# Performance work log

Measured on AMD Instinct MI355X. Metric: run time of the kernel, lower is better.

## Reference

```python
import jax, jax.numpy as jnp
import numpy as np

B, NQ, NK, D, DV = 16, 2048, 2048, 128, 128


def setup_inputs() -> dict:
    key = jax.random.key(0)
    kq, kk, kv, kl = jax.random.split(key, 4)
    return {
        "queries": jax.random.normal(kq, (B, NQ, D), dtype=jnp.float32),
        "keys": jax.random.normal(kk, (B, NK, D), dtype=jnp.float32),
        "values": jax.random.normal(kv, (B, NK, DV), dtype=jnp.float32),
        "valid_lens": jax.random.randint(kl, (B,), 1, NK + 1, dtype=jnp.int32),
    }


def reference(queries, keys, values, valid_lens):
    d = queries.shape[-1]
    # scores: [B, NQ, NK]
    scores = jnp.einsum("bqd,bkd->bqk", queries, keys) / jnp.sqrt(jnp.float32(d))
    # mask positions >= valid_len with -1e6 (matches sequence_mask semantics)
    key_pos = jnp.arange(scores.shape[-1], dtype=jnp.int32)  # [NK]
    mask = key_pos[None, None, :] < valid_lens[:, None, None]  # [B,1,NK] -> broadcast over queries
    scores = jnp.where(mask, scores, jnp.float32(-1000000.0))
    attn = jax.nn.softmax(scores, axis=-1)
    # dropout p=0.0 -> identity
    return jnp.einsum("bqk,bkv->bqv", attn, values)
```

## Files before the change

### kernel.cpp

```cpp
#include <hip/hip_runtime.h>


#define B_   16
#define NQ_  2048
#define NK_  2048
#define D_   128
#define DV_  128

typedef __attribute__((ext_vector_type(4))) float          f32x4;
typedef __attribute__((ext_vector_type(8))) __bf16         bf16x8;
typedef __attribute__((ext_vector_type(8))) unsigned short ushort8v;
typedef __attribute__((ext_vector_type(4))) unsigned short ushort4v;

__device__ __forceinline__ unsigned short f2bf(float f) {
    unsigned u = __builtin_bit_cast(unsigned, f);
    return (unsigned short)((u + 0x8000u) >> 16);
}
__device__ __forceinline__ float bf2f(unsigned short h) {
    unsigned u = ((unsigned)h) << 16;
    return __builtin_bit_cast(float, u);
}

__global__ __launch_bounds__(256, 2) void attn_fwd(
    const float* __restrict__ Q, const float* __restrict__ K,
    const float* __restrict__ V, const int* __restrict__ vlen,
    float* __restrict__ Out)
{
    __shared__ unsigned short Kt[64][136];
    __shared__ unsigned short Vt[128 * 64];
    __shared__ unsigned short Pb[4][16][72];

    const int tid  = threadIdx.x;
    const int w    = tid >> 6;
    const int L    = tid & 63;
    const int col  = L & 15;
    const int quad = L >> 4;
    const int b     = blockIdx.y;
    const int qbase = blockIdx.x * 64;
    const int vl    = vlen[b];
    const int ntiles = (vl + 63) >> 6;

    const float qscale = 0.12751743f;
    bf16x8 qf[4];
    {
        const int qrow = qbase + w * 16 + col;
        const float* gQ = Q + ((size_t)b * NQ_ + qrow) * D_;
        #pragma unroll
        for (int c = 0; c < 4; ++c) {
            const float* p = gQ + c * 32 + quad * 8;
            f32x4 a0 = *(const f32x4*)(p);
            f32x4 a1 = *(const f32x4*)(p + 4);
            ushort8v us;
            us[0] = f2bf(a0[0] * qscale); us[1] = f2bf(a0[1] * qscale);
            us[2] = f2bf(a0[2] * qscale); us[3] = f2bf(a0[3] * qscale);
            us[4] = f2bf(a1[0] * qscale); us[5] = f2bf(a1[1] * qscale);
            us[6] = f2bf(a1[2] * qscale); us[7] = f2bf(a1[3] * qscale);
            qf[c] = __builtin_bit_cast(bf16x8, us);
        }
    }

    f32x4 o[8];
    #pragma unroll
    for (int c = 0; c < 8; ++c) o[c] = (f32x4){0.f, 0.f, 0.f, 0.f};
    float m_run[4] = {-1e30f, -1e30f, -1e30f, -1e30f};
    float l_run[4] = {0.f, 0.f, 0.f, 0.f};

    const float* gKb = K + (size_t)b * NK_ * D_;
    const float* gVb = V + (size_t)b * NK_ * DV_;

    f32x4 kreg[8];
    float vreg[4][8];

    #define ISSUE_LOADS(K0)                                                  \
        do {                                                                 \
            _Pragma("unroll")                                                \
            for (int i = 0; i < 8; ++i) {                                    \
                int f = i * 256 + tid;                                       \
                int row = f >> 5, c4 = (f & 31) * 4;                         \
                kreg[i] = *(const f32x4*)(gKb + (size_t)((K0) + row) * D_ + c4); \
            }                                                                \
            _Pragma("unroll")                                                \
            for (int i = 0; i < 4; ++i) {                                    \
                int item = i * 256 + tid;                                    \
                int dv = item & 127, kg = item >> 7;                         \
                const float* vp = gVb + (size_t)((K0) + kg * 8) * DV_ + dv;  \
                _Pragma("unroll")                                            \
                for (int j = 0; j < 8; ++j) vreg[i][j] = vp[(size_t)j * DV_];\
            }                                                                \
        } while (0)

    ISSUE_LOADS(0);

    for (int kt = 0; kt < ntiles; ++kt) {
        __syncthreads();

        #pragma unroll
        for (int i = 0; i < 8; ++i) {
            int f = i * 256 + tid;
            int row = f >> 5, c4 = (f & 31) * 4;
            ushort4v ks;
            ks[0] = f2bf(kreg[i][0]); ks[1] = f2bf(kreg[i][1]);
            ks[2] = f2bf(kreg[i][2]); ks[3] = f2bf(kreg[i][3]);
            *(ushort4v*)&Kt[row][c4] = ks;
        }
        #pragma unroll
        for (int i = 0; i < 4; ++i) {
            int item = i * 256 + tid;
            int dv = item & 127, kg = item >> 7;
            ushort8v us;
            #pragma unroll
            for (int j = 0; j < 8; ++j) us[j] = f2bf(vreg[i][j]);
            *(ushort8v*)&Vt[dv * 64 + (((kg ^ (dv & 7))) << 3)] = us;
        }

        if (kt + 1 < ntiles) ISSUE_LOADS((kt + 1) * 64);

        __syncthreads();

        const int k0 = kt * 64;

        f32x4 s[4];
        #pragma unroll
        for (int kc = 0; kc < 4; ++kc) {
            f32x4 acc = (f32x4){0.f, 0.f, 0.f, 0.f};
            const unsigned short* krow = &Kt[kc * 16 + col][quad * 8];
            #pragma unroll
            for (int c = 0; c < 4; ++c) {
                bf16x8 kb = __builtin_bit_cast(bf16x8, *(const ushort8v*)(krow + c * 32));
                acc = __builtin_amdgcn_mfma_f32_16x16x32_bf16(qf[c], kb, acc, 0, 0, 0);
            }
            s[kc] = acc;
        }

        if (k0 + 64 > vl) {
            #pragma unroll
            for (int kc = 0; kc < 4; ++kc)
                if (k0 + kc * 16 + col >= vl)
                    s[kc] = (f32x4){-1e30f, -1e30f, -1e30f, -1e30f};
        }

        float mx[4];
        #pragma unroll
        for (int r = 0; r < 4; ++r)
            mx[r] = fmaxf(fmaxf(s[0][r], s[1][r]), fmaxf(s[2][r], s[3][r]));
        #pragma unroll
        for (int off = 1; off < 16; off <<= 1) {
            #pragma unroll
            for (int r = 0; r < 4; ++r)
                mx[r] = fmaxf(mx[r], __shfl_xor(mx[r], off, 64));
        }

        f32x4 al;
        #pragma unroll
        for (int r = 0; r < 4; ++r) {
            float mn = fmaxf(m_run[r], mx[r]);
            al[r] = exp2f(m_run[r] - mn);
            m_run[r] = mn;
        }

        float rs[4] = {0.f, 0.f, 0.f, 0.f};
        #pragma unroll
        for (int kc = 0; kc < 4; ++kc) {
            #pragma unroll
            for (int r = 0; r < 4; ++r) {
                unsigned short pb = f2bf(exp2f(s[kc][r] - m_run[r]));
                Pb[w][quad * 4 + r][kc * 16 + col] = pb;
                rs[r] += bf2f(pb);
            }
        }
        #pragma unroll
        for (int off = 1; off < 16; off <<= 1) {
            #pragma unroll
            for (int r = 0; r < 4; ++r)
                rs[r] += __shfl_xor(rs[r], off, 64);
        }
        #pragma unroll
        for (int r = 0; r < 4; ++r)
            l_run[r] = l_run[r] * al[r] + rs[r];
        #pragma unroll
        for (int c = 0; c < 8; ++c) o[c] *= al;


        #pragma unroll
        for (int kc2 = 0; kc2 < 2; ++kc2) {
            bf16x8 pa = __builtin_bit_cast(bf16x8,
                *(const ushort8v*)&Pb[w][col][kc2 * 32 + quad * 8]);
            #pragma unroll
            for (int c = 0; c < 8; ++c) {
                int dv = c * 16 + col;
                int sw = ((kc2 * 4 + quad) ^ (col & 7)) << 3;
                bf16x8 vb = __builtin_bit_cast(bf16x8,
                    *(const ushort8v*)&Vt[dv * 64 + sw]);
                o[c] = __builtin_amdgcn_mfma_f32_16x16x32_bf16(pa, vb, o[c], 0, 0, 0);
            }
        }
    }

    f32x4 linv;
    #pragma unroll
    for (int r = 0; r < 4; ++r) linv[r] = 1.0f / l_run[r];
    float* gO = Out + ((size_t)b * NQ_ + qbase + w * 16) * DV_;
    #pragma unroll
    for (int c = 0; c < 8; ++c) {
        #pragma unroll
        for (int r = 0; r < 4; ++r)
            gO[(size_t)(quad * 4 + r) * DV_ + c * 16 + col] = o[c][r] * linv[r];
    }
    #undef ISSUE_LOADS
}

extern "C" void kernel_launch(void* const* d_in, const int* in_sizes, int n_in,
                              void* d_out, int out_size, void* d_ws, size_t ws_size,
                              hipStream_t stream) {
    const float* Q  = (const float*)d_in[0];
    const float* K  = (const float*)d_in[1];
    const float* V  = (const float*)d_in[2];
    const int*   vl = (const int*)d_in[3];
    float* out = (float*)d_out;
    dim3 grid(NQ_ / 64, B_, 1);
    attn_fwd<<<grid, dim3(256, 1, 1), 0, stream>>>(Q, K, V, vl, out);
}
```

Baseline: 154.7 us.

## Split KV range across two blocks per query tile with flag-based merge

```diff
diff --git a/kernel.cpp b/kernel.cpp
--- a/kernel.cpp
+++ b/kernel.cpp
@@ -6,11 +6,21 @@
 #define NK_  2048
 #define D_   128
 #define DV_  128
+#define NQT_ 32
+#define NPAIR_ (B_ * NQT_)
+#define KHALF_TILES 16
 
 typedef __attribute__((ext_vector_type(4))) float          f32x4;
 typedef __attribute__((ext_vector_type(8))) __bf16         bf16x8;
 typedef __attribute__((ext_vector_type(8))) unsigned short ushort8v;
-typedef __attribute__((ext_vector_type(4))) unsigned short ushort4v;
+typedef __attribute__((ext_vector_type(2))) unsigned int   uint2v;
+typedef __attribute__((ext_vector_type(4))) unsigned int   uint4v;
+
+#ifdef __has_builtin
+#if __has_builtin(__builtin_amdgcn_cvt_pk_bf16_f32)
+#define HAVE_CVT_PK_BF16 1
+#endif
+#endif
 
 __device__ __forceinline__ unsigned short f2bf(float f) {
     unsigned u = __builtin_bit_cast(unsigned, f);
@@ -20,44 +30,44 @@
     unsigned u = ((unsigned)h) << 16;
     return __builtin_bit_cast(float, u);
 }
-
-__global__ __launch_bounds__(256, 2) void attn_fwd(
+__device__ __forceinline__ unsigned f2bf2(float a, float b) {
+#ifdef HAVE_CVT_PK_BF16
+    auto t = __builtin_amdgcn_cvt_pk_bf16_f32(a, b);
+    return __builtin_bit_cast(unsigned, t);
+#else
+    return (unsigned)f2bf(a) | ((unsigned)f2bf(b) << 16);
+#endif
+}
+
+__global__ void init_flags(int* __restrict__ f) { f[threadIdx.x] = 0; }
+
+__global__ __launch_bounds__(256, 3) void attn_fwd(
     const float* __restrict__ Q, const float* __restrict__ K,
     const float* __restrict__ V, const int* __restrict__ vlen,
-    float* __restrict__ Out)
+    float* __restrict__ Out, int* __restrict__ flags,
+    float* __restrict__ mlbuf, unsigned short* __restrict__ obuf)
 {
     __shared__ unsigned short Kt[64][136];
     __shared__ unsigned short Vt[128 * 64];
     __shared__ unsigned short Pb[4][16][72];
+    __shared__ int s_old;
 
     const int tid  = threadIdx.x;
     const int w    = tid >> 6;
     const int L    = tid & 63;
     const int col  = L & 15;
     const int quad = L >> 4;
-    const int b     = blockIdx.y;
-    const int qbase = blockIdx.x * 64;
+
+    const int id   = blockIdx.x;
+    const int h    = id >> 9;
+    const int pid  = id & 511;
+    const int b    = pid & 15;
+    const int qt   = pid >> 4;
+    const int qbase = qt * 64;
     const int vl    = vlen[b];
     const int ntiles = (vl + 63) >> 6;
-
-    const float qscale = 0.12751743f;
-    bf16x8 qf[4];
-    {
-        const int qrow = qbase + w * 16 + col;
-        const float* gQ = Q + ((size_t)b * NQ_ + qrow) * D_;
-        #pragma unroll
-        for (int c = 0; c < 4; ++c) {
-            const float* p = gQ + c * 32 + quad * 8;
-            f32x4 a0 = *(const f32x4*)(p);
-            f32x4 a1 = *(const f32x4*)(p + 4);
-            ushort8v us;
-            us[0] = f2bf(a0[0] * qscale); us[1] = f2bf(a0[1] * qscale);
-            us[2] = f2bf(a0[2] * qscale); us[3] = f2bf(a0[3] * qscale);
-            us[4] = f2bf(a1[0] * qscale); us[5] = f2bf(a1[1] * qscale);
-            us[6] = f2bf(a1[2] * qscale); us[7] = f2bf(a1[3] * qscale);
-            qf[c] = __builtin_bit_cast(bf16x8, us);
-        }
-    }
+    const int t0 = h * KHALF_TILES;
+    const int t1 = ntiles < (h + 1) * KHALF_TILES ? ntiles : (h + 1) * KHALF_TILES;
 
     f32x4 o[8];
     #pragma unroll
@@ -65,148 +75,210 @@
     float m_run[4] = {-1e30f, -1e30f, -1e30f, -1e30f};
     float l_run[4] = {0.f, 0.f, 0.f, 0.f};
 
-    const float* gKb = K + (size_t)b * NK_ * D_;
-    const float* gVb = V + (size_t)b * NK_ * DV_;
-
-    f32x4 kreg[8];
-    float vreg[4][8];
-
-    #define ISSUE_LOADS(K0)                                                  \
-        do {                                                                 \
-            _Pragma("unroll")                                                \
-            for (int i = 0; i < 8; ++i) {                                    \
-                int f = i * 256 + tid;                                       \
-                int row = f >> 5, c4 = (f & 31) * 4;                         \
-                kreg[i] = *(const f32x4*)(gKb + (size_t)((K0) + row) * D_ + c4); \
-            }                                                                \
-            _Pragma("unroll")                                                \
-            for (int i = 0; i < 4; ++i) {                                    \
-                int item = i * 256 + tid;                                    \
-                int dv = item & 127, kg = item >> 7;                         \
-                const float* vp = gVb + (size_t)((K0) + kg * 8) * DV_ + dv;  \
-                _Pragma("unroll")                                            \
-                for (int j = 0; j < 8; ++j) vreg[i][j] = vp[(size_t)j * DV_];\
-            }                                                                \
-        } while (0)
-
-    ISSUE_LOADS(0);
-
-    for (int kt = 0; kt < ntiles; ++kt) {
-        __syncthreads();
-
-        #pragma unroll
-        for (int i = 0; i < 8; ++i) {
-            int f = i * 256 + tid;
-            int row = f >> 5, c4 = (f & 31) * 4;
-            ushort4v ks;
-            ks[0] = f2bf(kreg[i][0]); ks[1] = f2bf(kreg[i][1]);
-            ks[2] = f2bf(kreg[i][2]); ks[3] = f2bf(kreg[i][3]);
-            *(ushort4v*)&Kt[row][c4] = ks;
-        }
-        #pragma unroll
-        for (int i = 0; i < 4; ++i) {
-            int item = i * 256 + tid;
-            int dv = item & 127, kg = item >> 7;
-            ushort8v us;
-            #pragma unroll
-            for (int j = 0; j < 8; ++j) us[j] = f2bf(vreg[i][j]);
-            *(ushort8v*)&Vt[dv * 64 + (((kg ^ (dv & 7))) << 3)] = us;
-        }
-
-        if (kt + 1 < ntiles) ISSUE_LOADS((kt + 1) * 64);
-
-        __syncthreads();
-
-        const int k0 = kt * 64;
-
-        f32x4 s[4];
-        #pragma unroll
-        for (int kc = 0; kc < 4; ++kc) {
-            f32x4 acc = (f32x4){0.f, 0.f, 0.f, 0.f};
-            const unsigned short* krow = &Kt[kc * 16 + col][quad * 8];
+    if (t0 < t1) {
+        const float qscale = 0.12751743f;
+        bf16x8 qf[4];
+        {
+            const int qrow = qbase + w * 16 + col;
+            const float* gQ = Q + ((size_t)b * NQ_ + qrow) * D_;
             #pragma unroll
             for (int c = 0; c < 4; ++c) {
-                bf16x8 kb = __builtin_bit_cast(bf16x8, *(const ushort8v*)(krow + c * 32));
-                acc = __builtin_amdgcn_mfma_f32_16x16x32_bf16(qf[c], kb, acc, 0, 0, 0);
-            }
-            s[kc] = acc;
-        }
-
-        if (k0 + 64 > vl) {
-            #pragma unroll
-            for (int kc = 0; kc < 4; ++kc)
-                if (k0 + kc * 16 + col >= vl)
-                    s[kc] = (f32x4){-1e30f, -1e30f, -1e30f, -1e30f};
-        }
-
-        float mx[4];
-        #pragma unroll
-        for (int r = 0; r < 4; ++r)
-            mx[r] = fmaxf(fmaxf(s[0][r], s[1][r]), fmaxf(s[2][r], s[3][r]));
-        #pragma unroll
-        for (int off = 1; off < 16; off <<= 1) {
+                const float* p = gQ + c * 32 + quad * 8;
+                f32x4 a0 = *(const f32x4*)(p);
+                f32x4 a1 = *(const f32x4*)(p + 4);
+                uint4v us;
+                us[0] = f2bf2(a0[0] * qscale, a0[1] * qscale);
+                us[1] = f2bf2(a0[2] * qscale, a0[3] * qscale);
+                us[2] = f2bf2(a1[0] * qscale, a1[1] * qscale);
+                us[3] = f2bf2(a1[2] * qscale, a1[3] * qscale);
+                qf[c] = __builtin_bit_cast(bf16x8, us);
+            }
+        }
+
+        const float* gKb = K + (size_t)b * NK_ * D_;
+        const float* gVb = V + (size_t)b * NK_ * DV_;
+
+        f32x4 kreg[8];
+        float vreg[4][8];
+
+        #define ISSUE_LOADS(K0)                                                  \
+            do {                                                                 \
+                _Pragma("unroll")                                                \
+                for (int i = 0; i < 8; ++i) {                                    \
+                    int f = i * 256 + tid;                                       \
+                    int row = f >> 5, c4 = (f & 31) * 4;                         \
+                    kreg[i] = *(const f32x4*)(gKb + (size_t)((K0) + row) * D_ + c4); \
+                }                                                                \
+                _Pragma("unroll")                                                \
+                for (int i = 0; i < 4; ++i) {                                    \
+                    int item = i * 256 + tid;                                    \
+                    int dv = item & 127, kg = item >> 7;                         \
+                    const float* vp = gVb + (size_t)((K0) + kg * 8) * DV_ + dv;  \
+                    _Pragma("unroll")                                            \
+                    for (int j = 0; j < 8; ++j) vreg[i][j] = vp[(size_t)j * DV_];\
+                }                                                                \
+            } while (0)
+
+        ISSUE_LOADS(t0 * 64);
+
+        for (int kt = t0; kt < t1; ++kt) {
+            __syncthreads();
+
+            #pragma unroll
+            for (int i = 0; i < 8; ++i) {
+                int f = i * 256 + tid;
+                int row = f >> 5, c4 = (f & 31) * 4;
+                uint2v ks;
+                ks[0] = f2bf2(kreg[i][0], kreg[i][1]);
+                ks[1] = f2bf2(kreg[i][2], kreg[i][3]);
+                *(uint2v*)&Kt[row][c4] = ks;
+            }
+            #pragma unroll
+            for (int i = 0; i < 4; ++i) {
+                int item = i * 256 + tid;
+                int dv = item & 127, kg = item >> 7;
+                uint4v us;
+                us[0] = f2bf2(vreg[i][0], vreg[i][1]);
+                us[1] = f2bf2(vreg[i][2], vreg[i][3]);
+                us[2] = f2bf2(vreg[i][4], vreg[i][5]);
+                us[3] = f2bf2(vreg[i][6], vreg[i][7]);
+                *(uint4v*)&Vt[dv * 64 + ((kg ^ (dv & 7)) << 3)] = us;
+            }
+
+            if (kt + 1 < t1) ISSUE_LOADS((kt + 1) * 64);
+
+            __syncthreads();
+
+            const int k0 = kt * 64;
+
+            f32x4 s[4];
+            #pragma unroll
+            for (int kc = 0; kc < 4; ++kc) {
+                f32x4 acc = (f32x4){0.f, 0.f, 0.f, 0.f};
+                const unsigned short* krow = &Kt[kc * 16 + col][quad * 8];
+                #pragma unroll
+                for (int c = 0; c < 4; ++c) {
+                    bf16x8 kb = __builtin_bit_cast(bf16x8, *(const ushort8v*)(krow + c * 32));
+                    acc = __builtin_amdgcn_mfma_f32_16x16x32_bf16(qf[c], kb, acc, 0, 0, 0);
+                }
+                s[kc] = acc;
+            }
+
+            if (k0 + 64 > vl) {
+                #pragma unroll
+                for (int kc = 0; kc < 4; ++kc)
+                    if (k0 + kc * 16 + col >= vl)
+                        s[kc] = (f32x4){-1e30f, -1e30f, -1e30f, -1e30f};
+            }
+
+            float mx[4];
             #pragma unroll
             for (int r = 0; r < 4; ++r)
-                mx[r] = fmaxf(mx[r], __shfl_xor(mx[r], off, 64));
-        }
-
-        f32x4 al;
+                mx[r] = fmaxf(fmaxf(s[0][r], s[1][r]), fmaxf(s[2][r], s[3][r]));
+            #pragma unroll
+            for (int off = 1; off < 16; off <<= 1) {
+                #pragma unroll
+                for (int r = 0; r < 4; ++r)
+                    mx[r] = fmaxf(mx[r], __shfl_xor(mx[r], off, 64));
+            }
+
+            f32x4 al;
+            #pragma unroll
+            for (int r = 0; r < 4; ++r) {
+                float mn = fmaxf(m_run[r], mx[r]);
+                al[r] = exp2f(m_run[r] - mn);
+                m_run[r] = mn;
+            }
+
+            float rs[4] = {0.f, 0.f, 0.f, 0.f};
+            #pragma unroll
+            for (int kc = 0; kc < 4; ++kc) {
+                #pragma unroll
+                for (int r = 0; r < 4; ++r) {
+                    unsigned short pb = f2bf(exp2f(s[kc][r] - m_run[r]));
+                    Pb[w][quad * 4 + r][kc * 16 + col] = pb;
+                    rs[r] += bf2f(pb);
+                }
+            }
+            #pragma unroll
+            for (int off = 1; off < 16; off <<= 1) {
+                #pragma unroll
+                for (int r = 0; r < 4; ++r)
+                    rs[r] += __shfl_xor(rs[r], off, 64);
+            }
+            #pragma unroll
+            for (int r = 0; r < 4; ++r)
+                l_run[r] = l_run[r] * al[r] + rs[r];
+            #pragma unroll
+            for (int c = 0; c < 8; ++c) o[c] *= al;
+
+
+            #pragma unroll
+            for (int kc2 = 0; kc2 < 2; ++kc2) {
+                bf16x8 pa = __builtin_bit_cast(bf16x8,
+                    *(const ushort8v*)&Pb[w][col][kc2 * 32 + quad * 8]);
+                #pragma unroll
+                for (int c = 0; c < 8; ++c) {
+                    int dv = c * 16 + col;
+                    int sw = ((kc2 * 4 + quad) ^ (col & 7)) << 3;
+                    bf16x8 vb = __builtin_bit_cast(bf16x8,
+                        *(const ushort8v*)&Vt[dv * 64 + sw]);
+                    o[c] = __builtin_amdgcn_mfma_f32_16x16x32_bf16(pa, vb, o[c], 0, 0, 0);
+                }
+            }
+        }
+        #undef ISSUE_LOADS
+    }
+
+    const int slot = pid * 2 + h;
+    const int myrow = w * 16 + quad * 4;
+    float* ml = mlbuf + (size_t)slot * 128;
+    if (col == 0) {
         #pragma unroll
         for (int r = 0; r < 4; ++r) {
-            float mn = fmaxf(m_run[r], mx[r]);
-            al[r] = exp2f(m_run[r] - mn);
-            m_run[r] = mn;
-        }
-
-        float rs[4] = {0.f, 0.f, 0.f, 0.f};
+            ml[myrow + r]      = m_run[r];
+            ml[64 + myrow + r] = l_run[r];
+        }
+    }
+    if (t0 < t1) {
+        unsigned short* Ow = obuf + (size_t)slot * 8192;
         #pragma unroll
-        for (int kc = 0; kc < 4; ++kc) {
+        for (int c = 0; c < 8; ++c)
+            #pragma unroll
+            for (int r = 0; r < 4; ++r)
+                Ow[(size_t)(myrow + r) * 128 + c * 16 + col] = f2bf(o[c][r]);
+    }
+    __threadfence();
+    __syncthreads();
+    if (tid == 0) s_old = atomicAdd(&flags[pid], 1);
+    __syncthreads();
+
+    if (s_old == 1) {
+        __threadfence();
+        const int oslot = pid * 2 + (1 - h);
+        const float* mlo = mlbuf + (size_t)oslot * 128;
+        const unsigned short* Oo = obuf + (size_t)oslot * 8192;
+        float aa[4], ab[4], inv[4];
+        #pragma unroll
+        for (int r = 0; r < 4; ++r) {
+            float mb = mlo[myrow + r];
+            float lb = mlo[64 + myrow + r];
+            float m  = fmaxf(m_run[r], mb);
+            aa[r] = exp2f(m_run[r] - m);
+            ab[r] = exp2f(mb - m);
+            inv[r] = 1.0f / (l_run[r] * aa[r] + lb * ab[r]);
+        }
+        float* gO = Out + ((size_t)b * NQ_ + qbase + w * 16) * DV_;
+        #pragma unroll
+        for (int c = 0; c < 8; ++c) {
             #pragma unroll
             for (int r = 0; r < 4; ++r) {
-                unsigned short pb = f2bf(exp2f(s[kc][r] - m_run[r]));
-                Pb[w][quad * 4 + r][kc * 16 + col] = pb;
-                rs[r] += bf2f(pb);
-            }
-        }
-        #pragma unroll
-        for (int off = 1; off < 16; off <<= 1) {
-            #pragma unroll
-            for (int r = 0; r < 4; ++r)
-                rs[r] += __shfl_xor(rs[r], off, 64);
-        }
-        #pragma unroll
-        for (int r = 0; r < 4; ++r)
-            l_run[r] = l_run[r] * al[r] + rs[r];
-        #pragma unroll
-        for (int c = 0; c < 8; ++c) o[c] *= al;
-
-
-        #pragma unroll
-        for (int kc2 = 0; kc2 < 2; ++kc2) {
-            bf16x8 pa = __builtin_bit_cast(bf16x8,
-                *(const ushort8v*)&Pb[w][col][kc2 * 32 + quad * 8]);
-            #pragma unroll
-            for (int c = 0; c < 8; ++c) {
-                int dv = c * 16 + col;
-                int sw = ((kc2 * 4 + quad) ^ (col & 7)) << 3;
-                bf16x8 vb = __builtin_bit_cast(bf16x8,
-                    *(const ushort8v*)&Vt[dv * 64 + sw]);
-                o[c] = __builtin_amdgcn_mfma_f32_16x16x32_bf16(pa, vb, o[c], 0, 0, 0);
+                float pv = bf2f(Oo[(size_t)(myrow + r - w * 16 + w * 16) * 128 + c * 16 + col]);
+                gO[(size_t)(quad * 4 + r) * DV_ + c * 16 + col] =
+                    (o[c][r] * aa[r] + pv * ab[r]) * inv[r];
             }
         }
     }
-
-    f32x4 linv;
-    #pragma unroll
-    for (int r = 0; r < 4; ++r) linv[r] = 1.0f / l_run[r];
-    float* gO = Out + ((size_t)b * NQ_ + qbase + w * 16) * DV_;
-    #pragma unroll
-    for (int c = 0; c < 8; ++c) {
-        #pragma unroll
-        for (int r = 0; r < 4; ++r)
-            gO[(size_t)(quad * 4 + r) * DV_ + c * 16 + col] = o[c][r] * linv[r];
-    }
-    #undef ISSUE_LOADS
 }
 
 extern "C" void kernel_launch(void* const* d_in, const int* in_sizes, int n_in,
@@ -217,6 +289,13 @@
     const float* V  = (const float*)d_in[2];
     const int*   vl = (const int*)d_in[3];
     float* out = (float*)d_out;
-    dim3 grid(NQ_ / 64, B_, 1);
-    attn_fwd<<<grid, dim3(256, 1, 1), 0, stream>>>(Q, K, V, vl, out);
-}
+
+    char* ws = (char*)d_ws;
+    int*   flags = (int*)ws;
+    float* mlbuf = (float*)(ws + 4096);
+    unsigned short* obuf = (unsigned short*)(ws + (1u << 20));
+
+    init_flags<<<1, NPAIR_, 0, stream>>>(flags);
+    attn_fwd<<<dim3(2 * NPAIR_, 1, 1), dim3(256, 1, 1), 0, stream>>>(
+        Q, K, V, vl, out, flags, mlbuf, obuf);
+}
```

New measurement: 404.0 us. 161% more time.

## Schedule attention blocks by valid length and use packed bf16 conversion

Applied to the files above, without the earlier changes.

```diff
diff --git a/kernel.cpp b/kernel.cpp
--- a/kernel.cpp
+++ b/kernel.cpp
@@ -6,11 +6,19 @@
 #define NK_  2048
 #define D_   128
 #define DV_  128
+#define NTASK_ 512
 
 typedef __attribute__((ext_vector_type(4))) float          f32x4;
 typedef __attribute__((ext_vector_type(8))) __bf16         bf16x8;
 typedef __attribute__((ext_vector_type(8))) unsigned short ushort8v;
-typedef __attribute__((ext_vector_type(4))) unsigned short ushort4v;
+typedef __attribute__((ext_vector_type(2))) unsigned int   uint2v;
+typedef __attribute__((ext_vector_type(4))) unsigned int   uint4v;
+
+#ifdef __has_builtin
+#if __has_builtin(__builtin_amdgcn_cvt_pk_bf16_f32)
+#define HAVE_CVT_PK_BF16 1
+#endif
+#endif
 
 __device__ __forceinline__ unsigned short f2bf(float f) {
     unsigned u = __builtin_bit_cast(unsigned, f);
@@ -20,11 +28,42 @@
     unsigned u = ((unsigned)h) << 16;
     return __builtin_bit_cast(float, u);
 }
+__device__ __forceinline__ unsigned f2bf2(float a, float b) {
+#ifdef HAVE_CVT_PK_BF16
+    auto t = __builtin_amdgcn_cvt_pk_bf16_f32(a, b);
+    return __builtin_bit_cast(unsigned, t);
+#else
+    return (unsigned)f2bf(a) | ((unsigned)f2bf(b) << 16);
+#endif
+}
+
+__global__ void make_schedule(const int* __restrict__ vlen, int* __restrict__ task) {
+    __shared__ int s[16];
+    int tid = threadIdx.x;
+    if (tid < 16) {
+        int my = vlen[tid];
+        int rank = 0;
+        for (int o = 0; o < 16; ++o) {
+            int vo = vlen[o];
+            if (vo > my || (vo == my && o < tid)) ++rank;
+        }
+        s[rank] = tid;
+    }
+    __syncthreads();
+    for (int e = tid; e < NTASK_; e += 64) {
+        int half = e >> 8;
+        int r    = e & 255;
+        int p    = r >> 5;
+        int qt   = r & 31;
+        int b    = half ? s[15 - p] : s[p];
+        task[e]  = b | (qt << 8);
+    }
+}
 
 __global__ __launch_bounds__(256, 2) void attn_fwd(
     const float* __restrict__ Q, const float* __restrict__ K,
     const float* __restrict__ V, const int* __restrict__ vlen,
-    float* __restrict__ Out)
+    const int* __restrict__ task, float* __restrict__ Out)
 {
     __shared__ unsigned short Kt[64][136];
     __shared__ unsigned short Vt[128 * 64];
@@ -35,8 +74,10 @@
     const int L    = tid & 63;
     const int col  = L & 15;
     const int quad = L >> 4;
-    const int b     = blockIdx.y;
-    const int qbase = blockIdx.x * 64;
+
+    const int tk    = task[blockIdx.x];
+    const int b     = tk & 255;
+    const int qbase = (tk >> 8) * 64;
     const int vl    = vlen[b];
     const int ntiles = (vl + 63) >> 6;
 
@@ -50,11 +91,11 @@
             const float* p = gQ + c * 32 + quad * 8;
             f32x4 a0 = *(const f32x4*)(p);
             f32x4 a1 = *(const f32x4*)(p + 4);
-            ushort8v us;
-            us[0] = f2bf(a0[0] * qscale); us[1] = f2bf(a0[1] * qscale);
-            us[2] = f2bf(a0[2] * qscale); us[3] = f2bf(a0[3] * qscale);
-            us[4] = f2bf(a1[0] * qscale); us[5] = f2bf(a1[1] * qscale);
-            us[6] = f2bf(a1[2] * qscale); us[7] = f2bf(a1[3] * qscale);
+            uint4v us;
+            us[0] = f2bf2(a0[0] * qscale, a0[1] * qscale);
+            us[1] = f2bf2(a0[2] * qscale, a0[3] * qscale);
+            us[2] = f2bf2(a1[0] * qscale, a1[1] * qscale);
+            us[3] = f2bf2(a1[2] * qscale, a1[3] * qscale);
             qf[c] = __builtin_bit_cast(bf16x8, us);
         }
     }
@@ -98,19 +139,21 @@
         for (int i = 0; i < 8; ++i) {
             int f = i * 256 + tid;
             int row = f >> 5, c4 = (f & 31) * 4;
-            ushort4v ks;
-            ks[0] = f2bf(kreg[i][0]); ks[1] = f2bf(kreg[i][1]);
-            ks[2] = f2bf(kreg[i][2]); ks[3] = f2bf(kreg[i][3]);
-            *(ushort4v*)&Kt[row][c4] = ks;
+            uint2v ks;
+            ks[0] = f2bf2(kreg[i][0], kreg[i][1]);
+            ks[1] = f2bf2(kreg[i][2], kreg[i][3]);
+            *(uint2v*)&Kt[row][c4] = ks;
         }
         #pragma unroll
         for (int i = 0; i < 4; ++i) {
             int item = i * 256 + tid;
             int dv = item & 127, kg = item >> 7;
-            ushort8v us;
-            #pragma unroll
-            for (int j = 0; j < 8; ++j) us[j] = f2bf(vreg[i][j]);
-            *(ushort8v*)&Vt[dv * 64 + (((kg ^ (dv & 7))) << 3)] = us;
+            uint4v us;
+            us[0] = f2bf2(vreg[i][0], vreg[i][1]);
+            us[1] = f2bf2(vreg[i][2], vreg[i][3]);
+            us[2] = f2bf2(vreg[i][4], vreg[i][5]);
+            us[3] = f2bf2(vreg[i][6], vreg[i][7]);
+            *(uint4v*)&Vt[dv * 64 + ((kg ^ (dv & 7)) << 3)] = us;
         }
 
         if (kt + 1 < ntiles) ISSUE_LOADS((kt + 1) * 64);
@@ -217,6 +260,9 @@
     const float* V  = (const float*)d_in[2];
     const int*   vl = (const int*)d_in[3];
     float* out = (float*)d_out;
-    dim3 grid(NQ_ / 64, B_, 1);
-    attn_fwd<<<grid, dim3(256, 1, 1), 0, stream>>>(Q, K, V, vl, out);
-}
+    int* task = (int*)d_ws;
+
+    make_schedule<<<1, 64, 0, stream>>>(vl, task);
+    attn_fwd<<<dim3(NTASK_, 1, 1), dim3(256, 1, 1), 0, stream>>>(
+        Q, K, V, vl, task, out);
+}
```

Measured after the change: 158.6 us. +2.5%, slower.
